# Kernel optimization log

Hardware: AMD Instinct MI355X
Metric: run time of the kernel (lower is better)

The kernel has to match this reference:

```python
import jax, jax.numpy as jnp
import numpy as np

N, M, E, D = 100000, 20000, 1600000, 128


def setup_inputs() -> dict:
    key = jax.random.key(0)
    ks = jax.random.split(key, 14)
    s = 1.0 / np.sqrt(D)
    inp = {
        "x": jax.random.normal(ks[0], (N, D), jnp.float32),
        "in_src": jax.random.randint(ks[1], (E,), 0, N),
        "in_dst": jax.random.randint(ks[2], (E,), 0, M),
        "has_src": jax.random.randint(ks[3], (E,), 0, M),
        "has_dst": jax.random.randint(ks[4], (E,), 0, N),
        "W1": jax.random.normal(ks[5], (D, D), jnp.float32) * s,
        "b1": jnp.zeros((D,), jnp.float32),
        "an1": jax.random.normal(ks[6], (D, 1), jnp.float32) * s,
        "ae1": jax.random.normal(ks[7], (D, 1), jnp.float32) * s,
        "W2": jax.random.normal(ks[8], (D, D), jnp.float32) * s,
        "b2": jnp.zeros((D,), jnp.float32),
        "an2": jax.random.normal(ks[9], (D, 1), jnp.float32) * s,
        "ae2": jax.random.normal(ks[10], (D, 1), jnp.float32) * s,
    }
    return inp


def _hgat_layer(x, W, b, an, ae, in_src, in_dst, has_src, has_dst, activate):
    h = x @ W + b                       # [N, D] fc transform
    n_attn = h @ an                     # [N, 1] node attn scores
    # node -> hyperedge ('in' edges). h_e is unset at this point (local_scope),
    # so the hyperedge bias term is zero; e = attn[src].
    e = n_attn[in_src]                  # [E, 1]
    # source uses F.softmax(e, dim=0): GLOBAL softmax over all edges
    attn = jax.nn.softmax(e, axis=0)    # [E, 1]
    h_e = jax.ops.segment_sum(attn * h[in_src], in_dst, num_segments=M)  # [M, D]
    e_attn = h_e @ ae                   # [M, 1] hyperedge attn scores
    # hyperedge -> node ('has' edges): bias is node attn score at dst
    e2 = e_attn[has_src] + n_attn[has_dst]  # [E, 1]
    attn2 = jax.nn.softmax(e2, axis=0)      # global softmax over all edges
    h_n = jax.ops.segment_sum(attn2 * h_e[has_src], has_dst, num_segments=N)  # [N, D]
    return jax.nn.relu(h_n) if activate else h_n


def reference(x, in_src, in_dst, has_src, has_dst,
              W1, b1, an1, ae1, W2, b2, an2, ae2):
    # layer 1 (activation=relu), layer 2 (no activation); dropout in eval mode
    h = _hgat_layer(x, W1, b1, an1, ae1, in_src, in_dst, has_src, has_dst, True)
    h = _hgat_layer(h, W2, b2, an2, ae2, in_src, in_dst, has_src, has_dst, False)
    return h
```

## Files before the change

### kernel.cpp

```cpp
#include <hip/hip_runtime.h>
#include <hip/hip_bf16.h>
#include <math.h>


typedef unsigned int u32;
typedef unsigned short u16;
typedef u16 u16x8 __attribute__((ext_vector_type(8)));
typedef short bf16x8 __attribute__((ext_vector_type(8)));
typedef float f32x4 __attribute__((ext_vector_type(4)));

#define NCONST 100000
#define MCONST 20000
#define ECONST 1600000
#define HCH 16384
#define HBC 32

#define PBLK 256
#define PT 6250
#define SHB_IN 6
#define NBK_IN 313
#define SRCB_IN 17
#define SHB_HAS 8
#define NBK_HAS 391
#define SRCB_HAS 15

__device__ __forceinline__ u16 f2bf(float f) {
  u32 u = __float_as_uint(f);
  u += 0x7FFFu + ((u >> 16) & 1u);
  return (u16)(u >> 16);
}
__device__ __forceinline__ float bf2f(u16 b) {
  return __uint_as_float(((u32)b) << 16);
}

__global__ __launch_bounds__(256) void k_hpart(const int* __restrict__ arr, int n,
                                               int* __restrict__ partial) {
  __shared__ int hc[HCH];
  int lo = blockIdx.y * HCH;
  for (int i = threadIdx.x; i < HCH; i += 256) hc[i] = 0;
  __syncthreads();
  int stride = gridDim.x * 256;
  int n4 = n >> 2;
  const int4* a4 = (const int4*)arr;
  for (int i = blockIdx.x * 256 + threadIdx.x; i < n4; i += stride) {
    int4 v = a4[i];
    u32 a = (u32)(v.x - lo), b = (u32)(v.y - lo), c = (u32)(v.z - lo), d = (u32)(v.w - lo);
    if (a < HCH) atomicAdd(&hc[a], 1);
    if (b < HCH) atomicAdd(&hc[b], 1);
    if (c < HCH) atomicAdd(&hc[c], 1);
    if (d < HCH) atomicAdd(&hc[d], 1);
  }
  for (int i = (n4 << 2) + blockIdx.x * 256 + threadIdx.x; i < n; i += stride) {
    u32 v = (u32)(arr[i] - lo);
    if (v < HCH) atomicAdd(&hc[v], 1);
  }
  __syncthreads();
  int* out = partial + ((size_t)blockIdx.y * gridDim.x + blockIdx.x) * HCH;
  for (int i = threadIdx.x; i < HCH; i += 256) out[i] = hc[i];
}

__global__ void k_hred(const int* __restrict__ partial, int range, int* __restrict__ cnt) {
  int j = blockIdx.x * 256 + threadIdx.x;
  if (j >= range) return;
  int chunk = j / HCH, jloc = j & (HCH - 1);
  const int* p = partial + (size_t)chunk * HBC * HCH + jloc;
  int s = 0;
#pragma unroll
  for (int b = 0; b < HBC; ++b) s += p[(size_t)b * HCH];
  cnt[j] = s;
}

__global__ void k_scan1(const int* __restrict__ cnt, int n, int* __restrict__ off,
                        int* __restrict__ bsum) {
  __shared__ int sd[256];
  int t = threadIdx.x;
  int base = blockIdx.x * 1024 + t * 4;
  int v0 = (base + 0 < n) ? cnt[base + 0] : 0;
  int v1 = (base + 1 < n) ? cnt[base + 1] : 0;
  int v2 = (base + 2 < n) ? cnt[base + 2] : 0;
  int v3 = (base + 3 < n) ? cnt[base + 3] : 0;
  v1 += v0; v2 += v1; v3 += v2;
  int tot = v3;
  sd[t] = tot;
  __syncthreads();
  for (int o = 1; o < 256; o <<= 1) {
    int x = (t >= o) ? sd[t - o] : 0;
    __syncthreads();
    sd[t] += x;
    __syncthreads();
  }
  int excl = sd[t] - tot;
  if (base + 0 < n) off[base + 1] = v0 + excl;
  if (base + 1 < n) off[base + 2] = v1 + excl;
  if (base + 2 < n) off[base + 3] = v2 + excl;
  if (base + 3 < n) off[base + 4] = v3 + excl;
  if (t == 255) bsum[blockIdx.x] = sd[255];
}

__global__ void k_scan2(int* __restrict__ bsum, int nb) {
  __shared__ int sd[256];
  int t = threadIdx.x;
  int v = (t < nb) ? bsum[t] : 0;
  sd[t] = v;
  __syncthreads();
  for (int o = 1; o < 256; o <<= 1) {
    int x = (t >= o) ? sd[t - o] : 0;
    __syncthreads();
    sd[t] += x;
    __syncthreads();
  }
  if (t < nb) bsum[t] = sd[t] - v;
}

__global__ void k_scan3(int* __restrict__ off, int n, const int* __restrict__ bsum) {
  int i = blockIdx.x * blockDim.x + threadIdx.x;
  int st = gridDim.x * blockDim.x;
  if (blockIdx.x == 0 && threadIdx.x == 0) off[0] = 0;
  for (; i < n; i += st) off[i + 1] += bsum[i >> 10];
}

__global__ __launch_bounds__(256) void k_coarse(const int* __restrict__ in_dst,
                                                const int* __restrict__ has_dst,
                                                int* __restrict__ bb_in,
                                                int* __restrict__ bb_has) {
  __shared__ int h1[NBK_IN];
  __shared__ int h2[NBK_HAS];
  for (int i = threadIdx.x; i < NBK_IN; i += 256) h1[i] = 0;
  for (int i = threadIdx.x; i < NBK_HAS; i += 256) h2[i] = 0;
  __syncthreads();
  int c0 = blockIdx.x * PT, c1 = min(c0 + PT, ECONST);
  for (int i = c0 + threadIdx.x; i < c1; i += 256) {
    atomicAdd(&h1[in_dst[i] >> SHB_IN], 1);
    atomicAdd(&h2[has_dst[i] >> SHB_HAS], 1);
  }
  __syncthreads();
  int* o1 = bb_in + (size_t)blockIdx.x * NBK_IN;
  for (int i = threadIdx.x; i < NBK_IN; i += 256) o1[i] = h1[i];
  int* o2 = bb_has + (size_t)blockIdx.x * NBK_HAS;
  for (int i = threadIdx.x; i < NBK_HAS; i += 256) o2[i] = h2[i];
}

__global__ __launch_bounds__(256) void k_colscan(int* __restrict__ bb, int nbuk,
                                                 const int* __restrict__ off, int shb,
                                                 int segs) {
  __shared__ int sd[256];
  int b = blockIdx.x;
  int t = threadIdx.x;
  int v = bb[(size_t)t * nbuk + b];
  sd[t] = v;
  __syncthreads();
  for (int o = 1; o < 256; o <<= 1) {
    int x = (t >= o) ? sd[t - o] : 0;
    __syncthreads();
    sd[t] += x;
    __syncthreads();
  }
  bb[(size_t)t * nbuk + b] = sd[t] - v + off[min(b << shb, segs)];
}

template <int NBUK, int SHB, int SRCB>
__global__ __launch_bounds__(256) void k_stage(const int* __restrict__ dst,
                                               const int* __restrict__ srcv,
                                               const int* __restrict__ bb,
                                               int* __restrict__ ebuf) {
  __shared__ int hist[NBUK];
  __shared__ int loff[NBUK];
  __shared__ int gbase[NBUK];
  __shared__ int stage[PT];
  __shared__ int sd[256];
  int t = threadIdx.x;
  for (int i = t; i < NBUK; i += 256) hist[i] = 0;
  __syncthreads();
  int c0 = blockIdx.x * PT, c1 = min(c0 + PT, ECONST);
  for (int i = c0 + t; i < c1; i += 256) atomicAdd(&hist[dst[i] >> SHB], 1);
  __syncthreads();
  {
    int v0 = (2 * t < NBUK) ? hist[2 * t] : 0;
    int v1 = (2 * t + 1 < NBUK) ? hist[2 * t + 1] : 0;
    sd[t] = v0 + v1;
    __syncthreads();
    for (int o = 1; o < 256; o <<= 1) {
      int x = (t >= o) ? sd[t - o] : 0;
      __syncthreads();
      sd[t] += x;
      __syncthreads();
    }
    int excl = sd[t] - (v0 + v1);
    if (2 * t < NBUK) loff[2 * t] = excl;
    if (2 * t + 1 < NBUK) loff[2 * t + 1] = excl + v0;
  }
  __syncthreads();
  for (int i = t; i < NBUK; i += 256) {
    gbase[i] = bb[(size_t)blockIdx.x * NBUK + i];
    hist[i] = loff[i];
  }
  __syncthreads();
  for (int i = c0 + t; i < c1; i += 256) {
    int d = dst[i], s = srcv[i];
    int b = d >> SHB;
    int r = atomicAdd(&hist[b], 1);
    stage[r] = (b << 23) | ((d & ((1 << SHB) - 1)) << SRCB) | s;
  }
  __syncthreads();
  int tot = c1 - c0;
  for (int i = t; i < tot; i += 256) {
    int v = stage[i];
    int b = ((u32)v) >> 23;
    ebuf[gbase[b] + (i - loff[b])] = v & ((1 << 23) - 1);
  }
}

template <int SHB, int SRCB>
__global__ __launch_bounds__(256) void k_place(const int* __restrict__ off, int segs,
                                               const int* __restrict__ ebuf,
                                               int* __restrict__ csrc) {
  const int NSEG = 1 << SHB;
  __shared__ int cur[NSEG];
  int seg0 = blockIdx.x << SHB;
  if (seg0 >= segs) return;
  int segN = min(seg0 + NSEG, segs);
  for (int i = threadIdx.x; i < segN - seg0; i += 256) cur[i] = off[seg0 + i];
  __syncthreads();
  int start = off[seg0], end = off[segN];
  for (int i = start + threadIdx.x; i < end; i += 256) {
    int v = ebuf[i];
    int dloc = ((u32)v) >> SRCB;
    int pos = atomicAdd(&cur[dloc], 1);
    csrc[pos] = v & ((1 << SRCB) - 1);
  }
}

__global__ __launch_bounds__(256, 2) void k_fc(
    const float* __restrict__ x, const float* __restrict__ W,
    const float* __restrict__ bias, const float* __restrict__ an,
    u16* __restrict__ h, float* __restrict__ na, int nrows) {
  __shared__ __align__(16) u16 sWT[128 * 136];
  int tid = threadIdx.x;
  int lane = tid & 63, w = tid >> 6;
  int cl = lane & 15, qg = lane >> 4;

  for (int i = tid * 4; i < 16384; i += 1024) {
    float4 v = *(const float4*)(W + i);
    int k = i >> 7, j = i & 127;
    sWT[(j + 0) * 136 + k] = f2bf(v.x);
    sWT[(j + 1) * 136 + k] = f2bf(v.y);
    sWT[(j + 2) * 136 + k] = f2bf(v.z);
    sWT[(j + 3) * 136 + k] = f2bf(v.w);
  }

  float anv[8], bv[8];
#pragma unroll
  for (int t = 0; t < 8; ++t) {
    anv[t] = an[t * 16 + cl];
    bv[t] = bias[t * 16 + cl];
  }

  int rbase = blockIdx.x * 128 + w * 32;
  bf16x8 afr[2][4];
#pragma unroll
  for (int g = 0; g < 2; ++g) {
    int r = rbase + g * 16 + cl;
    int rc = min(r, nrows - 1);
    const float* xp = x + (size_t)rc * 128 + qg * 8;
#pragma unroll
    for (int s = 0; s < 4; ++s) {
      float4 u0 = *(const float4*)(xp + s * 32);
      float4 u1 = *(const float4*)(xp + s * 32 + 4);
      bf16x8 a;
      a[0] = (short)f2bf(u0.x); a[1] = (short)f2bf(u0.y);
      a[2] = (short)f2bf(u0.z); a[3] = (short)f2bf(u0.w);
      a[4] = (short)f2bf(u1.x); a[5] = (short)f2bf(u1.y);
      a[6] = (short)f2bf(u1.z); a[7] = (short)f2bf(u1.w);
      afr[g][s] = a;
    }
  }
  __syncthreads();

  f32x4 acc[2][8];
#pragma unroll
  for (int g = 0; g < 2; ++g)
#pragma unroll
    for (int t = 0; t < 8; ++t) {
      acc[g][t][0] = 0.f; acc[g][t][1] = 0.f; acc[g][t][2] = 0.f; acc[g][t][3] = 0.f;
    }

#pragma unroll
  for (int t = 0; t < 8; ++t) {
    bf16x8 bfrg[4];
    const u16* bp = sWT + (t * 16 + cl) * 136 + qg * 8;
#pragma unroll
    for (int s = 0; s < 4; ++s) bfrg[s] = *(const bf16x8*)(bp + s * 32);
#pragma unroll
    for (int s = 0; s < 4; ++s) {
#pragma unroll
      for (int g = 0; g < 2; ++g)
        acc[g][t] = __builtin_amdgcn_mfma_f32_16x16x32_bf16(afr[g][s], bfrg[s], acc[g][t],
                                                            0, 0, 0);
    }
  }

  float pa[2][4];
#pragma unroll
  for (int g = 0; g < 2; ++g)
#pragma unroll
    for (int reg = 0; reg < 4; ++reg) pa[g][reg] = 0.f;
#pragma unroll
  for (int g = 0; g < 2; ++g)
#pragma unroll
    for (int t = 0; t < 8; ++t)
#pragma unroll
      for (int reg = 0; reg < 4; ++reg)
        pa[g][reg] = fmaf(acc[g][t][reg] + bv[t], anv[t], pa[g][reg]);
#pragma unroll
  for (int g = 0; g < 2; ++g)
#pragma unroll
    for (int reg = 0; reg < 4; ++reg) {
      float v = pa[g][reg];
      v += __shfl_xor(v, 1, 64);
      v += __shfl_xor(v, 2, 64);
      v += __shfl_xor(v, 4, 64);
      v += __shfl_xor(v, 8, 64);
      pa[g][reg] = v;
    }
  if (cl == 0) {
#pragma unroll
    for (int g = 0; g < 2; ++g)
#pragma unroll
      for (int reg = 0; reg < 4; ++reg) {
        int r = rbase + g * 16 + qg * 4 + reg;
        if (r < nrows) na[r] = pa[g][reg];
      }
  }

  __syncthreads();
  u16* st = sWT + w * 32 * 136;
#pragma unroll
  for (int g = 0; g < 2; ++g)
#pragma unroll
    for (int t = 0; t < 8; ++t)
#pragma unroll
      for (int reg = 0; reg < 4; ++reg)
        st[(g * 16 + qg * 4 + reg) * 136 + t * 16 + cl] = f2bf(acc[g][t][reg] + bv[t]);
#pragma unroll
  for (int it = 0; it < 8; ++it) {
    int idx = it * 64 + lane;
    int row = idx >> 4, c = idx & 15;
    u16x8 v = *(const u16x8*)(st + row * 136 + c * 8);
    int r = rbase + row;
    if (r < nrows) *(u16x8*)(h + (size_t)r * 128 + c * 8) = v;
  }
}

__device__ __forceinline__ void merge_write(float m, float s, float2* __restrict__ pairs) {
  for (int o = 1; o < 64; o <<= 1) {
    float om = __shfl_xor(m, o, 64), os = __shfl_xor(s, o, 64);
    float nm = fmaxf(m, om);
    s = s * __expf(m - nm) + os * __expf(om - nm);
    m = nm;
  }
  __shared__ float sm[4], ss[4];
  int t = threadIdx.x;
  if ((t & 63) == 0) { sm[t >> 6] = m; ss[t >> 6] = s; }
  __syncthreads();
  if (t == 0) {
    for (int k = 1; k < 4; ++k) {
      float nm = fmaxf(m, sm[k]);
      s = s * __expf(m - nm) + ss[k] * __expf(sm[k] - nm);
      m = nm;
    }
    pairs[blockIdx.x] = make_float2(m, s);
  }
}

__global__ void k_sm1(const float* __restrict__ na, const int* __restrict__ deg, int n,
                      float2* __restrict__ pairs) {
  float m = -1e30f, s = 0.f;
  int i = blockIdx.x * blockDim.x + threadIdx.x;
  int st = gridDim.x * blockDim.x;
  for (; i < n; i += st) {
    int d = deg[i];
    if (d > 0) {
      float xv = na[i];
      if (xv > m) { s *= __expf(m - xv); m = xv; }
      s += (float)d * __expf(xv - m);
    }
  }
  merge_write(m, s, pairs);
}

__global__ void k_sm2(const float* __restrict__ ea, const float* __restrict__ na,
                      const int* __restrict__ hs, const int* __restrict__ hd, int n,
                      float2* __restrict__ pairs) {
  float m = -1e30f, s = 0.f;
  int i = blockIdx.x * blockDim.x + threadIdx.x;
  int st = gridDim.x * blockDim.x;
  for (; i < n; i += st) {
    float xv = ea[hs[i]] + na[hd[i]];
    if (xv > m) { s *= __expf(m - xv); m = xv; }
    s += __expf(xv - m);
  }
  merge_write(m, s, pairs);
}

__global__ void k_smfin(const float2* __restrict__ pairs, int nb, float* __restrict__ out) {
  int t = threadIdx.x;
  float m = -1e30f, s = 0.f;
  for (int i = t; i < nb; i += 256) {
    float2 pr = pairs[i];
    float nm = fmaxf(m, pr.x);
    s = s * __expf(m - nm) + pr.y * __expf(pr.x - nm);
    m = nm;
  }
  for (int o = 1; o < 64; o <<= 1) {
    float om = __shfl_xor(m, o, 64), os = __shfl_xor(s, o, 64);
    float nm = fmaxf(m, om);
    s = s * __expf(m - nm) + os * __expf(om - nm);
    m = nm;
  }
  __shared__ float sm[4], ss[4];
  if ((t & 63) == 0) { sm[t >> 6] = m; ss[t >> 6] = s; }
  __syncthreads();
  if (t == 0) {
    for (int k = 1; k < 4; ++k) {
      float nm = fmaxf(m, sm[k]);
      s = s * __expf(m - nm) + ss[k] * __expf(sm[k] - nm);
      m = nm;
    }
    out[0] = m;
    out[1] = s;
  }
}

__global__ void k_wnode(const float* __restrict__ na, const float* __restrict__ sc,
                        float* __restrict__ w, int n) {
  float mx = sc[0];
  float iz = 1.0f / sc[1];
  int i = blockIdx.x * blockDim.x + threadIdx.x;
  if (i < n) w[i] = __expf(na[i] - mx) * iz;
}

__global__ void k_pe(const float* __restrict__ ea, const float* __restrict__ sc,
                     float* __restrict__ pe, int m) {
  float mx = sc[0];
  float iz = 1.0f / sc[1];
  int i = blockIdx.x * blockDim.x + threadIdx.x;
  if (i < m) pe[i] = __expf(ea[i] - mx) * iz;
}

__global__ __launch_bounds__(256) void k_segA(
    const u16* __restrict__ h, const float* __restrict__ w,
    const int* __restrict__ csrc, const int* __restrict__ off,
    const float* __restrict__ ae, u16* __restrict__ he,
    float* __restrict__ ea, int m_count) {
  int wid = (blockIdx.x << 2) + (threadIdx.x >> 6);
  if (wid >= m_count) return;
  int lane = threadIdx.x & 63;
  int sub = lane >> 4, cl = lane & 15;
  int s = off[wid], t = off[wid + 1];
  float ax[8];
#pragma unroll
  for (int j = 0; j < 8; ++j) ax[j] = 0.f;
  for (int i = s + sub; i < t; i += 4) {
    int sr = csrc[i];
    float ww = w[sr];
    u16x8 v = *(const u16x8*)(h + (size_t)sr * 128 + cl * 8);
#pragma unroll
    for (int j = 0; j < 8; ++j) ax[j] = fmaf(ww, bf2f(v[j]), ax[j]);
  }
#pragma unroll
  for (int j = 0; j < 8; ++j) {
    ax[j] += __shfl_xor(ax[j], 16, 64);
    ax[j] += __shfl_xor(ax[j], 32, 64);
  }
  float4 a0 = *(const float4*)(ae + cl * 8);
  float4 a1 = *(const float4*)(ae + cl * 8 + 4);
  float pa = ax[0] * a0.x + ax[1] * a0.y + ax[2] * a0.z + ax[3] * a0.w +
             ax[4] * a1.x + ax[5] * a1.y + ax[6] * a1.z + ax[7] * a1.w;
  pa += __shfl_xor(pa, 1, 64);
  pa += __shfl_xor(pa, 2, 64);
  pa += __shfl_xor(pa, 4, 64);
  pa += __shfl_xor(pa, 8, 64);
  if (sub == 0) {
    u16x8 o;
#pragma unroll
    for (int j = 0; j < 8; ++j) o[j] = f2bf(ax[j]);
    *(u16x8*)(he + (size_t)wid * 128 + cl * 8) = o;
    if (cl == 0) ea[wid] = pa;
  }
}

__global__ __launch_bounds__(256) void k_segB(
    const u16* __restrict__ he, const float* __restrict__ pe,
    const float* __restrict__ na, const int* __restrict__ csrc,
    const int* __restrict__ off, float* __restrict__ y, int n_count, int relu) {
  int wid = (blockIdx.x << 2) + (threadIdx.x >> 6);
  if (wid >= n_count) return;
  int lane = threadIdx.x & 63;
  int sub = lane >> 4, cl = lane & 15;
  float rf = __expf(na[wid]);
  int s = off[wid], t = off[wid + 1];
  float ax[8];
#pragma unroll
  for (int j = 0; j < 8; ++j) ax[j] = 0.f;
  for (int i = s + sub; i < t; i += 4) {
    int sr = csrc[i];
    float c = pe[sr];
    u16x8 v = *(const u16x8*)(he + (size_t)sr * 128 + cl * 8);
#pragma unroll
    for (int j = 0; j < 8; ++j) ax[j] = fmaf(c, bf2f(v[j]), ax[j]);
  }
#pragma unroll
  for (int j = 0; j < 8; ++j) {
    ax[j] += __shfl_xor(ax[j], 16, 64);
    ax[j] += __shfl_xor(ax[j], 32, 64);
    ax[j] *= rf;
    if (relu) ax[j] = fmaxf(ax[j], 0.f);
  }
  if (sub == 0) {
    float4 A = make_float4(ax[0], ax[1], ax[2], ax[3]);
    float4 B = make_float4(ax[4], ax[5], ax[6], ax[7]);
    *(float4*)(y + (size_t)wid * 128 + cl * 8) = A;
    *(float4*)(y + (size_t)wid * 128 + cl * 8 + 4) = B;
  }
}

extern "C" void kernel_launch(void* const* d_in, const int* in_sizes, int n_in,
                              void* d_out, int out_size, void* d_ws, size_t ws_size,
                              hipStream_t stream) {
  const int N = NCONST, M = MCONST, E = ECONST;
  const float* x = (const float*)d_in[0];
  const int* in_src = (const int*)d_in[1];
  const int* in_dst = (const int*)d_in[2];
  const int* has_src = (const int*)d_in[3];
  const int* has_dst = (const int*)d_in[4];
  const float* W1 = (const float*)d_in[5];
  const float* b1 = (const float*)d_in[6];
  const float* an1 = (const float*)d_in[7];
  const float* ae1 = (const float*)d_in[8];
  const float* W2 = (const float*)d_in[9];
  const float* b2 = (const float*)d_in[10];
  const float* an2 = (const float*)d_in[11];
  const float* ae2 = (const float*)d_in[12];

  const int NCH_M = (MCONST + HCH - 1) / HCH;
  const int NCH_N = (NCONST + HCH - 1) / HCH;
  const size_t PARTIAL_BYTES = (size_t)NCH_N * HBC * HCH * 4;

  char* p = (char*)d_ws;
  auto alloc = [&](size_t bytes) {
    char* q = p;
    p += (bytes + 255) & ~(size_t)255;
    return q;
  };
  u16* h = (u16*)alloc((size_t)N * 128 * 2);
  u16* he = (u16*)alloc((size_t)M * 128 * 2);
  float* na = (float*)alloc((size_t)N * 4);
  float* ea = (float*)alloc((size_t)M * 4);
  float* wn = (float*)alloc((size_t)N * 4);
  float* pe = (float*)alloc((size_t)M * 4);
  int* off_in = (int*)alloc((size_t)(M + 1) * 4);
  int* off_has = (int*)alloc((size_t)(N + 1) * 4);
  int* csrc_in = (int*)alloc((size_t)E * 4);
  int* csrc_has = (int*)alloc((size_t)E * 4);
  int* partial = (int*)alloc(PARTIAL_BYTES);
  int* ebuf = partial;
  int* bb_in = (int*)alloc((size_t)PBLK * NBK_IN * 4);
  int* bb_has = (int*)alloc((size_t)PBLK * NBK_HAS * 4);
  int* bsum = (int*)alloc(256 * 4);
  float2* pairs = (float2*)alloc(256 * 8);
  float* scal = (float*)alloc(64);
  int* cnt_in = (int*)alloc((size_t)M * 4);
  int* cnt_has = (int*)alloc((size_t)N * 4);
  int* deg_src = (int*)alloc((size_t)N * 4);
  if ((size_t)(p - (char*)d_ws) > ws_size) return;

  k_hpart<<<dim3(HBC, NCH_M), 256, 0, stream>>>(in_dst, E, partial);
  k_hred<<<(M + 255) / 256, 256, 0, stream>>>(partial, M, cnt_in);
  k_hpart<<<dim3(HBC, NCH_N), 256, 0, stream>>>(has_dst, E, partial);
  k_hred<<<(N + 255) / 256, 256, 0, stream>>>(partial, N, cnt_has);
  k_hpart<<<dim3(HBC, NCH_N), 256, 0, stream>>>(in_src, E, partial);
  k_hred<<<(N + 255) / 256, 256, 0, stream>>>(partial, N, deg_src);

  int nb_in = (M + 1023) / 1024;
  k_scan1<<<nb_in, 256, 0, stream>>>(cnt_in, M, off_in, bsum);
  k_scan2<<<1, 256, 0, stream>>>(bsum, nb_in);
  k_scan3<<<256, 256, 0, stream>>>(off_in, M, bsum);
  int nb_has = (N + 1023) / 1024;
  k_scan1<<<nb_has, 256, 0, stream>>>(cnt_has, N, off_has, bsum);
  k_scan2<<<1, 256, 0, stream>>>(bsum, nb_has);
  k_scan3<<<512, 256, 0, stream>>>(off_has, N, bsum);

  k_coarse<<<PBLK, 256, 0, stream>>>(in_dst, has_dst, bb_in, bb_has);
  k_colscan<<<NBK_IN, 256, 0, stream>>>(bb_in, NBK_IN, off_in, SHB_IN, M);
  k_colscan<<<NBK_HAS, 256, 0, stream>>>(bb_has, NBK_HAS, off_has, SHB_HAS, N);
  k_stage<NBK_IN, SHB_IN, SRCB_IN><<<PBLK, 256, 0, stream>>>(in_dst, in_src, bb_in, ebuf);
  k_place<SHB_IN, SRCB_IN><<<NBK_IN, 256, 0, stream>>>(off_in, M, ebuf, csrc_in);
  k_stage<NBK_HAS, SHB_HAS, SRCB_HAS><<<PBLK, 256, 0, stream>>>(has_dst, has_src, bb_has,
                                                                ebuf);
  k_place<SHB_HAS, SRCB_HAS><<<NBK_HAS, 256, 0, stream>>>(off_has, N, ebuf, csrc_has);

  auto layer = [&](const float* xin, const float* W, const float* b, const float* an_,
                   const float* ae_, float* yout, int relu) {
    k_fc<<<(N + 127) / 128, 256, 0, stream>>>(xin, W, b, an_, h, na, N);
    k_sm1<<<256, 256, 0, stream>>>(na, deg_src, N, pairs);
    k_smfin<<<1, 256, 0, stream>>>(pairs, 256, scal);
    k_wnode<<<(N + 255) / 256, 256, 0, stream>>>(na, scal, wn, N);
    k_segA<<<(M + 3) / 4, 256, 0, stream>>>(h, wn, csrc_in, off_in, ae_, he, ea, M);
    k_sm2<<<256, 256, 0, stream>>>(ea, na, has_src, has_dst, E, pairs);
    k_smfin<<<1, 256, 0, stream>>>(pairs, 256, scal + 2);
    k_pe<<<(M + 255) / 256, 256, 0, stream>>>(ea, scal + 2, pe, M);
    k_segB<<<(N + 3) / 4, 256, 0, stream>>>(he, pe, na, csrc_has, off_has, yout, N, relu);
  };

  layer(x, W1, b1, an1, ae1, (float*)d_out, 1);
  layer((const float*)d_out, W2, b2, an2, ae2, (float*)d_out, 0);
}
```

Before: 532.9 us.

## Fuse histogram/scan passes, inline softmax weights, and store layer-1 output as bf16

Merges the in_dst and has_dst histograms into one kernel with larger shared-memory chunks and folds the partial-histogram reduction into a dual scan, cutting many small launches. The src-degree histogram is removed; the first softmax is now computed directly over edges by gathering na[in_src]. The per-node and per-hyperedge weight kernels (k_wnode, k_pe) are dropped and their exponentials are computed inline inside the segment kernels. Layer-1 output is written as bf16 and read directly by the second fc, halving that intermediate traffic. The trade-offs are extra exp work and random gathers over E edges, plus one more rounding step on the layer-1 activations.

```diff
diff --git a/kernel.cpp b/kernel.cpp
--- a/kernel.cpp
+++ b/kernel.cpp
@@ -12,8 +12,9 @@
 #define NCONST 100000
 #define MCONST 20000
 #define ECONST 1600000
-#define HCH 16384
+#define HCH2 32768
 #define HBC 32
+#define NCH_N 4
 
 #define PBLK 256
 #define PT 6250
@@ -33,54 +34,58 @@
   return __uint_as_float(((u32)b) << 16);
 }
 
-__global__ __launch_bounds__(256) void k_hpart(const int* __restrict__ arr, int n,
-                                               int* __restrict__ partial) {
-  __shared__ int hc[HCH];
-  int lo = blockIdx.y * HCH;
-  for (int i = threadIdx.x; i < HCH; i += 256) hc[i] = 0;
+__global__ __launch_bounds__(256) void k_hpart2(const int* __restrict__ in_dst,
+                                                const int* __restrict__ has_dst,
+                                                int* __restrict__ partial) {
+  __shared__ int hc[HCH2];
+  int y = blockIdx.y;
+  const int* __restrict__ arr = (y == 0) ? in_dst : has_dst;
+  int lo = (y == 0) ? 0 : (y - 1) * HCH2;
+  for (int i = threadIdx.x; i < HCH2; i += 256) hc[i] = 0;
   __syncthreads();
   int stride = gridDim.x * 256;
-  int n4 = n >> 2;
+  int n4 = ECONST >> 2;
   const int4* a4 = (const int4*)arr;
   for (int i = blockIdx.x * 256 + threadIdx.x; i < n4; i += stride) {
     int4 v = a4[i];
     u32 a = (u32)(v.x - lo), b = (u32)(v.y - lo), c = (u32)(v.z - lo), d = (u32)(v.w - lo);
-    if (a < HCH) atomicAdd(&hc[a], 1);
-    if (b < HCH) atomicAdd(&hc[b], 1);
-    if (c < HCH) atomicAdd(&hc[c], 1);
-    if (d < HCH) atomicAdd(&hc[d], 1);
-  }
-  for (int i = (n4 << 2) + blockIdx.x * 256 + threadIdx.x; i < n; i += stride) {
-    u32 v = (u32)(arr[i] - lo);
-    if (v < HCH) atomicAdd(&hc[v], 1);
-  }
-  __syncthreads();
-  int* out = partial + ((size_t)blockIdx.y * gridDim.x + blockIdx.x) * HCH;
-  for (int i = threadIdx.x; i < HCH; i += 256) out[i] = hc[i];
-}
-
-__global__ void k_hred(const int* __restrict__ partial, int range, int* __restrict__ cnt) {
-  int j = blockIdx.x * 256 + threadIdx.x;
-  if (j >= range) return;
-  int chunk = j / HCH, jloc = j & (HCH - 1);
-  const int* p = partial + (size_t)chunk * HBC * HCH + jloc;
-  int s = 0;
-#pragma unroll
-  for (int b = 0; b < HBC; ++b) s += p[(size_t)b * HCH];
-  cnt[j] = s;
-}
-
-__global__ void k_scan1(const int* __restrict__ cnt, int n, int* __restrict__ off,
-                        int* __restrict__ bsum) {
+    if (a < HCH2) atomicAdd(&hc[a], 1);
+    if (b < HCH2) atomicAdd(&hc[b], 1);
+    if (c < HCH2) atomicAdd(&hc[c], 1);
+    if (d < HCH2) atomicAdd(&hc[d], 1);
+  }
+  __syncthreads();
+  int* out = partial + ((size_t)y * HBC + blockIdx.x) * HCH2;
+  for (int i = threadIdx.x; i < HCH2; i += 256) out[i] = hc[i];
+}
+
+__global__ void k_scan1d(const int* __restrict__ partial, int nM, int nN,
+                         int* __restrict__ off_in, int* __restrict__ off_has,
+                         int* __restrict__ bsum) {
   __shared__ int sd[256];
+  int y = blockIdx.y;
+  int n = y ? nN : nM;
+  int yoff = y;
+  int* off = y ? off_has : off_in;
+  int* bs = bsum + y * 128;
   int t = threadIdx.x;
   int base = blockIdx.x * 1024 + t * 4;
-  int v0 = (base + 0 < n) ? cnt[base + 0] : 0;
-  int v1 = (base + 1 < n) ? cnt[base + 1] : 0;
-  int v2 = (base + 2 < n) ? cnt[base + 2] : 0;
-  int v3 = (base + 3 < n) ? cnt[base + 3] : 0;
-  v1 += v0; v2 += v1; v3 += v2;
-  int tot = v3;
+  int v[4];
+#pragma unroll
+  for (int k = 0; k < 4; ++k) {
+    int j = base + k;
+    int s = 0;
+    if (j < n) {
+      int chunk = j >> 15;
+      int jl = j & (HCH2 - 1);
+      const int* p = partial + ((size_t)(yoff + chunk) * HBC) * HCH2 + jl;
+#pragma unroll
+      for (int b = 0; b < HBC; ++b) s += p[(size_t)b * HCH2];
+    }
+    v[k] = s;
+  }
+  v[1] += v[0]; v[2] += v[1]; v[3] += v[2];
+  int tot = v[3];
   sd[t] = tot;
   __syncthreads();
   for (int o = 1; o < 256; o <<= 1) {
@@ -90,17 +95,18 @@
     __syncthreads();
   }
   int excl = sd[t] - tot;
-  if (base + 0 < n) off[base + 1] = v0 + excl;
-  if (base + 1 < n) off[base + 2] = v1 + excl;
-  if (base + 2 < n) off[base + 3] = v2 + excl;
-  if (base + 3 < n) off[base + 4] = v3 + excl;
-  if (t == 255) bsum[blockIdx.x] = sd[255];
-}
-
-__global__ void k_scan2(int* __restrict__ bsum, int nb) {
+#pragma unroll
+  for (int k = 0; k < 4; ++k)
+    if (base + k < n) off[base + k + 1] = v[k] + excl;
+  if (t == 255) bs[blockIdx.x] = sd[255];
+}
+
+__global__ void k_scan2d(int* __restrict__ bsum, int nbM, int nbN) {
   __shared__ int sd[256];
+  int* bs = bsum + blockIdx.x * 128;
+  int nb = blockIdx.x ? nbN : nbM;
   int t = threadIdx.x;
-  int v = (t < nb) ? bsum[t] : 0;
+  int v = (t < nb) ? bs[t] : 0;
   sd[t] = v;
   __syncthreads();
   for (int o = 1; o < 256; o <<= 1) {
@@ -109,14 +115,19 @@
     sd[t] += x;
     __syncthreads();
   }
-  if (t < nb) bsum[t] = sd[t] - v;
-}
-
-__global__ void k_scan3(int* __restrict__ off, int n, const int* __restrict__ bsum) {
+  if (t < nb) bs[t] = sd[t] - v;
+}
+
+__global__ void k_scan3d(int* __restrict__ off_in, int* __restrict__ off_has,
+                         const int* __restrict__ bsum, int nM, int nN) {
+  int y = blockIdx.y;
+  int* off = y ? off_has : off_in;
+  const int* bs = bsum + y * 128;
+  int n = y ? nN : nM;
   int i = blockIdx.x * blockDim.x + threadIdx.x;
   int st = gridDim.x * blockDim.x;
   if (blockIdx.x == 0 && threadIdx.x == 0) off[0] = 0;
-  for (; i < n; i += st) off[i + 1] += bsum[i >> 10];
+  for (; i < n; i += st) off[i + 1] += bs[i >> 10];
 }
 
 __global__ __launch_bounds__(256) void k_coarse(const int* __restrict__ in_dst,
@@ -230,8 +241,9 @@
   }
 }
 
+template <typename IT>
 __global__ __launch_bounds__(256, 2) void k_fc(
-    const float* __restrict__ x, const float* __restrict__ W,
+    const IT* __restrict__ x, const float* __restrict__ W,
     const float* __restrict__ bias, const float* __restrict__ an,
     u16* __restrict__ h, float* __restrict__ na, int nrows) {
   __shared__ __align__(16) u16 sWT[128 * 136];
@@ -261,17 +273,21 @@
   for (int g = 0; g < 2; ++g) {
     int r = rbase + g * 16 + cl;
     int rc = min(r, nrows - 1);
-    const float* xp = x + (size_t)rc * 128 + qg * 8;
+    const IT* xp = x + (size_t)rc * 128 + qg * 8;
 #pragma unroll
     for (int s = 0; s < 4; ++s) {
-      float4 u0 = *(const float4*)(xp + s * 32);
-      float4 u1 = *(const float4*)(xp + s * 32 + 4);
-      bf16x8 a;
-      a[0] = (short)f2bf(u0.x); a[1] = (short)f2bf(u0.y);
-      a[2] = (short)f2bf(u0.z); a[3] = (short)f2bf(u0.w);
-      a[4] = (short)f2bf(u1.x); a[5] = (short)f2bf(u1.y);
-      a[6] = (short)f2bf(u1.z); a[7] = (short)f2bf(u1.w);
-      afr[g][s] = a;
+      if constexpr (sizeof(IT) == 4) {
+        float4 u0 = *(const float4*)(xp + s * 32);
+        float4 u1 = *(const float4*)(xp + s * 32 + 4);
+        bf16x8 a;
+        a[0] = (short)f2bf(u0.x); a[1] = (short)f2bf(u0.y);
+        a[2] = (short)f2bf(u0.z); a[3] = (short)f2bf(u0.w);
+        a[4] = (short)f2bf(u1.x); a[5] = (short)f2bf(u1.y);
+        a[6] = (short)f2bf(u1.z); a[7] = (short)f2bf(u1.w);
+        afr[g][s] = a;
+      } else {
+        afr[g][s] = *(const bf16x8*)(xp + s * 32);
+      }
     }
   }
   __syncthreads();
@@ -372,18 +388,15 @@
   }
 }
 
-__global__ void k_sm1(const float* __restrict__ na, const int* __restrict__ deg, int n,
-                      float2* __restrict__ pairs) {
+__global__ void k_sm1e(const float* __restrict__ na, const int* __restrict__ src, int n,
+                       float2* __restrict__ pairs) {
   float m = -1e30f, s = 0.f;
   int i = blockIdx.x * blockDim.x + threadIdx.x;
   int st = gridDim.x * blockDim.x;
   for (; i < n; i += st) {
-    int d = deg[i];
-    if (d > 0) {
-      float xv = na[i];
-      if (xv > m) { s *= __expf(m - xv); m = xv; }
-      s += (float)d * __expf(xv - m);
-    }
+    float xv = na[src[i]];
+    if (xv > m) { s *= __expf(m - xv); m = xv; }
+    s += __expf(xv - m);
   }
   merge_write(m, s, pairs);
 }
@@ -431,29 +444,15 @@
   }
 }
 
-__global__ void k_wnode(const float* __restrict__ na, const float* __restrict__ sc,
-                        float* __restrict__ w, int n) {
-  float mx = sc[0];
-  float iz = 1.0f / sc[1];
-  int i = blockIdx.x * blockDim.x + threadIdx.x;
-  if (i < n) w[i] = __expf(na[i] - mx) * iz;
-}
-
-__global__ void k_pe(const float* __restrict__ ea, const float* __restrict__ sc,
-                     float* __restrict__ pe, int m) {
-  float mx = sc[0];
-  float iz = 1.0f / sc[1];
-  int i = blockIdx.x * blockDim.x + threadIdx.x;
-  if (i < m) pe[i] = __expf(ea[i] - mx) * iz;
-}
-
 __global__ __launch_bounds__(256) void k_segA(
-    const u16* __restrict__ h, const float* __restrict__ w,
-    const int* __restrict__ csrc, const int* __restrict__ off,
-    const float* __restrict__ ae, u16* __restrict__ he,
+    const u16* __restrict__ h, const float* __restrict__ na,
+    const float* __restrict__ scal, const int* __restrict__ csrc,
+    const int* __restrict__ off, const float* __restrict__ ae, u16* __restrict__ he,
     float* __restrict__ ea, int m_count) {
   int wid = (blockIdx.x << 2) + (threadIdx.x >> 6);
   if (wid >= m_count) return;
+  float mx = scal[0];
+  float iz = 1.0f / scal[1];
   int lane = threadIdx.x & 63;
   int sub = lane >> 4, cl = lane & 15;
   int s = off[wid], t = off[wid + 1];
@@ -462,7 +461,7 @@
   for (int j = 0; j < 8; ++j) ax[j] = 0.f;
   for (int i = s + sub; i < t; i += 4) {
     int sr = csrc[i];
-    float ww = w[sr];
+    float ww = __expf(na[sr] - mx) * iz;
     u16x8 v = *(const u16x8*)(h + (size_t)sr * 128 + cl * 8);
 #pragma unroll
     for (int j = 0; j < 8; ++j) ax[j] = fmaf(ww, bf2f(v[j]), ax[j]);
@@ -489,22 +488,26 @@
   }
 }
 
+template <int L1>
 __global__ __launch_bounds__(256) void k_segB(
-    const u16* __restrict__ he, const float* __restrict__ pe,
-    const float* __restrict__ na, const int* __restrict__ csrc,
-    const int* __restrict__ off, float* __restrict__ y, int n_count, int relu) {
+    const u16* __restrict__ he, const float* __restrict__ ea,
+    const float* __restrict__ na, const float* __restrict__ scal,
+    const int* __restrict__ csrc, const int* __restrict__ off,
+    void* __restrict__ yout, int n_count) {
   int wid = (blockIdx.x << 2) + (threadIdx.x >> 6);
   if (wid >= n_count) return;
+  float mx2 = scal[2];
+  float iz2 = 1.0f / scal[3];
   int lane = threadIdx.x & 63;
   int sub = lane >> 4, cl = lane & 15;
-  float rf = __expf(na[wid]);
+  float nav = na[wid];
   int s = off[wid], t = off[wid + 1];
   float ax[8];
 #pragma unroll
   for (int j = 0; j < 8; ++j) ax[j] = 0.f;
   for (int i = s + sub; i < t; i += 4) {
     int sr = csrc[i];
-    float c = pe[sr];
+    float c = __expf(ea[sr] + nav - mx2) * iz2;
     u16x8 v = *(const u16x8*)(he + (size_t)sr * 128 + cl * 8);
 #pragma unroll
     for (int j = 0; j < 8; ++j) ax[j] = fmaf(c, bf2f(v[j]), ax[j]);
@@ -513,14 +516,21 @@
   for (int j = 0; j < 8; ++j) {
     ax[j] += __shfl_xor(ax[j], 16, 64);
     ax[j] += __shfl_xor(ax[j], 32, 64);
-    ax[j] *= rf;
-    if (relu) ax[j] = fmaxf(ax[j], 0.f);
+    if (L1) ax[j] = fmaxf(ax[j], 0.f);
   }
   if (sub == 0) {
-    float4 A = make_float4(ax[0], ax[1], ax[2], ax[3]);
-    float4 B = make_float4(ax[4], ax[5], ax[6], ax[7]);
-    *(float4*)(y + (size_t)wid * 128 + cl * 8) = A;
-    *(float4*)(y + (size_t)wid * 128 + cl * 8 + 4) = B;
+    if (L1) {
+      u16x8 o;
+#pragma unroll
+      for (int j = 0; j < 8; ++j) o[j] = f2bf(ax[j]);
+      *(u16x8*)((u16*)yout + (size_t)wid * 128 + cl * 8) = o;
+    } else {
+      float4 A = make_float4(ax[0], ax[1], ax[2], ax[3]);
+      float4 B = make_float4(ax[4], ax[5], ax[6], ax[7]);
+      float* y = (float*)yout;
+      *(float4*)(y + (size_t)wid * 128 + cl * 8) = A;
+      *(float4*)(y + (size_t)wid * 128 + cl * 8 + 4) = B;
+    }
   }
 }
 
@@ -542,9 +552,7 @@
   const float* an2 = (const float*)d_in[11];
   const float* ae2 = (const float*)d_in[12];
 
-  const int NCH_M = (MCONST + HCH - 1) / HCH;
-  const int NCH_N = (NCONST + HCH - 1) / HCH;
-  const size_t PARTIAL_BYTES = (size_t)NCH_N * HBC * HCH * 4;
+  const size_t PARTIAL_BYTES = (size_t)(1 + NCH_N) * HBC * HCH2 * 4;
 
   char* p = (char*)d_ws;
   auto alloc = [&](size_t bytes) {
@@ -556,8 +564,6 @@
   u16* he = (u16*)alloc((size_t)M * 128 * 2);
   float* na = (float*)alloc((size_t)N * 4);
   float* ea = (float*)alloc((size_t)M * 4);
-  float* wn = (float*)alloc((size_t)N * 4);
-  float* pe = (float*)alloc((size_t)M * 4);
   int* off_in = (int*)alloc((size_t)(M + 1) * 4);
   int* off_has = (int*)alloc((size_t)(N + 1) * 4);
   int* csrc_in = (int*)alloc((size_t)E * 4);
@@ -567,28 +573,17 @@
   int* bb_in = (int*)alloc((size_t)PBLK * NBK_IN * 4);
   int* bb_has = (int*)alloc((size_t)PBLK * NBK_HAS * 4);
   int* bsum = (int*)alloc(256 * 4);
-  float2* pairs = (float2*)alloc(256 * 8);
+  float2* pairs = (float2*)alloc(512 * 8);
   float* scal = (float*)alloc(64);
-  int* cnt_in = (int*)alloc((size_t)M * 4);
-  int* cnt_has = (int*)alloc((size_t)N * 4);
-  int* deg_src = (int*)alloc((size_t)N * 4);
   if ((size_t)(p - (char*)d_ws) > ws_size) return;
 
-  k_hpart<<<dim3(HBC, NCH_M), 256, 0, stream>>>(in_dst, E, partial);
-  k_hred<<<(M + 255) / 256, 256, 0, stream>>>(partial, M, cnt_in);
-  k_hpart<<<dim3(HBC, NCH_N), 256, 0, stream>>>(has_dst, E, partial);
-  k_hred<<<(N + 255) / 256, 256, 0, stream>>>(partial, N, cnt_has);
-  k_hpart<<<dim3(HBC, NCH_N), 256, 0, stream>>>(in_src, E, partial);
-  k_hred<<<(N + 255) / 256, 256, 0, stream>>>(partial, N, deg_src);
-
-  int nb_in = (M + 1023) / 1024;
-  k_scan1<<<nb_in, 256, 0, stream>>>(cnt_in, M, off_in, bsum);
-  k_scan2<<<1, 256, 0, stream>>>(bsum, nb_in);
-  k_scan3<<<256, 256, 0, stream>>>(off_in, M, bsum);
-  int nb_has = (N + 1023) / 1024;
-  k_scan1<<<nb_has, 256, 0, stream>>>(cnt_has, N, off_has, bsum);
-  k_scan2<<<1, 256, 0, stream>>>(bsum, nb_has);
-  k_scan3<<<512, 256, 0, stream>>>(off_has, N, bsum);
+  u16* y1b = (u16*)d_out;
+
+  k_hpart2<<<dim3(HBC, 1 + NCH_N), 256, 0, stream>>>(in_dst, has_dst, partial);
+  int nbM = (M + 1023) / 1024, nbN = (N + 1023) / 1024;
+  k_scan1d<<<dim3(nbN, 2), 256, 0, stream>>>(partial, M, N, off_in, off_has, bsum);
+  k_scan2d<<<2, 256, 0, stream>>>(bsum, nbM, nbN);
+  k_scan3d<<<dim3(512, 2), 256, 0, stream>>>(off_in, off_has, bsum, M, N);
 
   k_coarse<<<PBLK, 256, 0, stream>>>(in_dst, has_dst, bb_in, bb_has);
   k_colscan<<<NBK_IN, 256, 0, stream>>>(bb_in, NBK_IN, off_in, SHB_IN, M);
@@ -599,19 +594,25 @@
                                                                 ebuf);
   k_place<SHB_HAS, SRCB_HAS><<<NBK_HAS, 256, 0, stream>>>(off_has, N, ebuf, csrc_has);
 
-  auto layer = [&](const float* xin, const float* W, const float* b, const float* an_,
-                   const float* ae_, float* yout, int relu) {
-    k_fc<<<(N + 127) / 128, 256, 0, stream>>>(xin, W, b, an_, h, na, N);
-    k_sm1<<<256, 256, 0, stream>>>(na, deg_src, N, pairs);
-    k_smfin<<<1, 256, 0, stream>>>(pairs, 256, scal);
-    k_wnode<<<(N + 255) / 256, 256, 0, stream>>>(na, scal, wn, N);
-    k_segA<<<(M + 3) / 4, 256, 0, stream>>>(h, wn, csrc_in, off_in, ae_, he, ea, M);
+  auto layer = [&](auto xin, const float* W, const float* b, const float* an_,
+                   const float* ae_, auto seg_b) {
+    using IT = typename std::remove_pointer<decltype(xin)>::type;
+    k_fc<typename std::remove_const<IT>::type>
+        <<<(N + 127) / 128, 256, 0, stream>>>(xin, W, b, an_, h, na, N);
+    k_sm1e<<<512, 256, 0, stream>>>(na, in_src, E, pairs);
+    k_smfin<<<1, 256, 0, stream>>>(pairs, 512, scal);
+    k_segA<<<(M + 3) / 4, 256, 0, stream>>>(h, na, scal, csrc_in, off_in, ae_, he, ea, M);
     k_sm2<<<256, 256, 0, stream>>>(ea, na, has_src, has_dst, E, pairs);
     k_smfin<<<1, 256, 0, stream>>>(pairs, 256, scal + 2);
-    k_pe<<<(M + 255) / 256, 256, 0, stream>>>(ea, scal + 2, pe, M);
-    k_segB<<<(N + 3) / 4, 256, 0, stream>>>(he, pe, na, csrc_has, off_has, yout, N, relu);
+    seg_b();
   };
 
-  layer(x, W1, b1, an1, ae1, (float*)d_out, 1);
-  layer((const float*)d_out, W2, b2, an2, ae2, (float*)d_out, 0);
-}
+  layer((const float*)x, W1, b1, an1, ae1, [&] {
+    k_segB<1><<<(N + 3) / 4, 256, 0, stream>>>(he, ea, na, scal, csrc_has, off_has,
+                                               (void*)y1b, N);
+  });
+  layer((const u16*)y1b, W2, b2, an2, ae2, [&] {
+    k_segB<0><<<(N + 3) / 4, 256, 0, stream>>>(he, ea, na, scal, csrc_has, off_has,
+                                               d_out, N);
+  });
+}
```

After: 481.5 us. 1.11x faster.
